# Kernel optimization log

Hardware: AMD Instinct MI355X
Metric: run time of the kernel (lower is better)

## Reference

```python
import jax, jax.numpy as jnp
import numpy as np

D_MODEL = 1024
N_HEADS = 16
HEAD_DIM = D_MODEL // N_HEADS
D_FF = 4096
LN_EPS = 1e-5


def _layer_norm(x, gamma, beta):
    mu = jnp.mean(x, axis=-1, keepdims=True)
    var = jnp.var(x, axis=-1, keepdims=True)
    return (x - mu) * jax.lax.rsqrt(var + LN_EPS) * gamma + beta


def setup_inputs() -> dict:
    key = jax.random.key(0)
    ks = jax.random.split(key, 16)
    s = 1.0 / np.sqrt(D_MODEL)
    sf = 1.0 / np.sqrt(D_FF)
    return {
        "x": jax.random.normal(ks[0], (4, 2048, D_MODEL), dtype=jnp.float32),
        "w_q": jax.random.uniform(ks[1], (D_MODEL, D_MODEL), jnp.float32, -s, s),
        "b_q": jax.random.uniform(ks[2], (D_MODEL,), jnp.float32, -s, s),
        "w_k": jax.random.uniform(ks[3], (D_MODEL, D_MODEL), jnp.float32, -s, s),
        "b_k": jax.random.uniform(ks[4], (D_MODEL,), jnp.float32, -s, s),
        "w_v": jax.random.uniform(ks[5], (D_MODEL, D_MODEL), jnp.float32, -s, s),
        "b_v": jax.random.uniform(ks[6], (D_MODEL,), jnp.float32, -s, s),
        "w_o": jax.random.uniform(ks[7], (D_MODEL, D_MODEL), jnp.float32, -s, s),
        "b_o": jax.random.uniform(ks[8], (D_MODEL,), jnp.float32, -s, s),
        "ln1_g": jnp.ones((D_MODEL,), jnp.float32),
        "ln1_b": jnp.zeros((D_MODEL,), jnp.float32),
        "w1": jax.random.uniform(ks[9], (D_MODEL, D_FF), jnp.float32, -s, s),
        "b1": jax.random.uniform(ks[10], (D_FF,), jnp.float32, -s, s),
        "w2": jax.random.uniform(ks[11], (D_FF, D_MODEL), jnp.float32, -sf, sf),
        "b2": jax.random.uniform(ks[12], (D_MODEL,), jnp.float32, -sf, sf),
        "ln2_g": jnp.ones((D_MODEL,), jnp.float32),
        "ln2_b": jnp.zeros((D_MODEL,), jnp.float32),
    }


def reference(x, w_q, b_q, w_k, b_k, w_v, b_v, w_o, b_o,
              ln1_g, ln1_b, w1, b1, w2, b2, ln2_g, ln2_b):
    B, S, D = x.shape
    # projections -> [B, H, S, Hd]
    def split_heads(t):
        return t.reshape(B, S, N_HEADS, HEAD_DIM).transpose(0, 2, 1, 3)
    q = split_heads(x @ w_q + b_q)
    k = split_heads(x @ w_k + b_k)
    v = split_heads(x @ w_v + b_v)
    scale = jnp.float32(np.sqrt(HEAD_DIM))
    scores = jnp.einsum('bhqd,bhkd->bhqk', q, k) / scale
    attn = jax.nn.softmax(scores, axis=-1)  # dropout = identity in eval
    ctx = jnp.einsum('bhqk,bhkd->bhqd', attn, v)
    ctx = ctx.transpose(0, 2, 1, 3).reshape(B, S, D)
    attn_out = ctx @ w_o + b_o
    h = _layer_norm(x + attn_out, ln1_g, ln1_b)
    ffn = jax.nn.relu(h @ w1 + b1) @ w2 + b2
    return _layer_norm(h + ffn, ln2_g, ln2_b)
```

## Files before the change

kernel.cpp:

```cpp
#include <hip/hip_runtime.h>
#include <cstdint>
#include <cstddef>

typedef unsigned short u16;
typedef short s16x8 __attribute__((ext_vector_type(8)));
typedef unsigned short u16x8 __attribute__((ext_vector_type(8)));
typedef unsigned short u16x4 __attribute__((ext_vector_type(4)));
typedef float f32x4 __attribute__((ext_vector_type(4)));
typedef unsigned int u32x2 __attribute__((ext_vector_type(2)));

#define MFMA_BF16(a, b, c) __builtin_amdgcn_mfma_f32_16x16x32_bf16((a), (b), (c), 0, 0, 0)

__device__ __forceinline__ float b2f(u16 u) {
    union { unsigned int i; float f; } x;
    x.i = ((unsigned int)u) << 16;
    return x.f;
}
__device__ __forceinline__ u16 f2b(float f) {
    union { float f; unsigned int i; } x;
    x.f = f;
    return (u16)((x.i + 0x8000u) >> 16);
}
__device__ __forceinline__ float exp2_hw(float x) {
    float r;
    asm volatile("v_exp_f32 %0, %1" : "=v"(r) : "v"(x));
    return r;
}
__device__ __forceinline__ unsigned int cvt_pk_bf16(float lo, float hi) {
    unsigned int r;
    asm("v_cvt_pk_bf16_f32 %0, %1, %2" : "=v"(r) : "v"(lo), "v"(hi));
    return r;
}

__device__ __forceinline__ void gload_lds16(const u16* g, u16* l) {
    __builtin_amdgcn_global_load_lds((__attribute__((address_space(1))) void*)(g),
                                     (__attribute__((address_space(3))) void*)(l),
                                     16, 0, 0);
}

__device__ __forceinline__ void transpose_tile(const float* __restrict__ in,
                                               u16* __restrict__ out,
                                               int R, int C, int bx, int by) {
    __shared__ u16 t[64][68];
    const int tc = bx * 64, tr = by * 64;
    for (int i = 0; i < 16; i++) {
        int idx = threadIdx.x + i * 256;
        int r = idx >> 6, c = idx & 63;
        t[r][c] = f2b(in[(size_t)(tr + r) * C + tc + c]);
    }
    __syncthreads();
    for (int i = 0; i < 16; i++) {
        int idx = threadIdx.x + i * 256;
        int r = idx >> 6, c = idx & 63;
        out[(size_t)(tc + r) * R + tr + c] = t[c][r];
    }
}

__global__ __launch_bounds__(256)
void prep_all(const float* __restrict__ w_q, const float* __restrict__ w_k,
              const float* __restrict__ w_v, const float* __restrict__ w_o,
              const float* __restrict__ w1, const float* __restrict__ w2,
              const float* __restrict__ x,
              u16* __restrict__ wqkv_t, u16* __restrict__ wo_t,
              u16* __restrict__ w1_t, u16* __restrict__ w2_t,
              u16* __restrict__ x_bf) {
    const int id = blockIdx.x;
    if (id < 1024) {
        const int j = id >> 8, lid = id & 255;
        const float* in = (j == 0) ? w_q : (j == 1) ? w_k : (j == 2) ? w_v : w_o;
        u16* out = (j == 0) ? wqkv_t
                 : (j == 1) ? wqkv_t + 1024 * 1024
                 : (j == 2) ? wqkv_t + 2 * 1024 * 1024
                 : wo_t;
        transpose_tile(in, out, 1024, 1024, lid & 15, lid >> 4);
    } else if (id < 2048) {
        const int lid = id - 1024;
        transpose_tile(w1, w1_t, 1024, 4096, lid & 63, lid >> 6);
    } else if (id < 3072) {
        const int lid = id - 2048;
        transpose_tile(w2, w2_t, 4096, 1024, lid & 15, lid >> 4);
    } else {
        const int i = ((id - 3072) * 256 + threadIdx.x) * 8;
        float4 a = *(const float4*)(x + i);
        float4 b = *(const float4*)(x + i + 4);
        u16x8 o;
        o[0] = f2b(a.x); o[1] = f2b(a.y); o[2] = f2b(a.z); o[3] = f2b(a.w);
        o[4] = f2b(b.x); o[5] = f2b(b.y); o[6] = f2b(b.z); o[7] = f2b(b.w);
        *(u16x8*)(x_bf + i) = o;
    }
}

enum { EPI_PLAIN = 0, EPI_RELU = 1, EPI_QKV = 2 };
#define SC_QK 0.1803368801111204f

template <int EPI>
__global__ __launch_bounds__(256, 3)
void gemm_bt(const u16* __restrict__ A, const u16* __restrict__ Bt,
             const float* __restrict__ bias0, const float* __restrict__ bias1,
             const float* __restrict__ bias2,
             u16* __restrict__ C0, u16* __restrict__ C1, u16* __restrict__ C2,
             int M, int N, int K) {
    __shared__ u16 As[128 * 64];
    __shared__ u16 Bs[128 * 64];
    const int tid = threadIdx.x;
    const int lane = tid & 63;
    const int wave = tid >> 6;
    const int qd = lane >> 4, cl = lane & 15;
    const int wr = (wave >> 1) * 64, wc = (wave & 1) * 64;
    const int m0 = blockIdx.x * 128, n0 = blockIdx.y * 128;

    const u16* AgP[4];
    const u16* BgP[4];
    int dsto[4];
    for (int c = 0; c < 4; c++) {
        const int d = tid * 8 + c * 2048;
        const int row = d >> 6;
        const int sblk = ((d >> 3) & 7) ^ (row & 7);
        AgP[c] = A + (size_t)(m0 + row) * K + sblk * 8;
        BgP[c] = Bt + (size_t)(n0 + row) * K + sblk * 8;
        dsto[c] = d;
    }

    const f32x4 Z = {0.f, 0.f, 0.f, 0.f};
    f32x4 acc[4][4];
    for (int i = 0; i < 4; i++)
        for (int j = 0; j < 4; j++) acc[i][j] = Z;

    for (int k = 0; k < K; k += 64) {
        __syncthreads();
        for (int c = 0; c < 4; c++) {
            gload_lds16(AgP[c] + k, As + dsto[c]);
            gload_lds16(BgP[c] + k, Bs + dsto[c]);
        }
        __syncthreads();
        for (int kk = 0; kk < 2; kk++) {
            s16x8 af[4], bfr[4];
            for (int i = 0; i < 4; i++) {
                const int row = wr + i * 16 + cl;
                af[i] = *(const s16x8*)(As + row * 64 +
                                        (((kk << 2) | qd) ^ (row & 7)) * 8);
            }
            for (int j = 0; j < 4; j++) {
                const int row = wc + j * 16 + cl;
                bfr[j] = *(const s16x8*)(Bs + row * 64 +
                                         (((kk << 2) | qd) ^ (row & 7)) * 8);
            }
            for (int i = 0; i < 4; i++)
                for (int j = 0; j < 4; j++)
                    acc[i][j] = MFMA_BF16(af[i], bfr[j], acc[i][j]);
        }
    }

    for (int j = 0; j < 4; j++) {
        const int col = n0 + wc + j * 16 + cl;
        float bv;
        if (EPI == EPI_QKV) {
            const int t = col >> 10, nn = col & 1023;
            const float* bp = (t == 0) ? bias0 : ((t == 1) ? bias1 : bias2);
            bv = bp[nn];
        } else {
            bv = bias0[col];
        }
        if (EPI == EPI_QKV && (col >> 10) == 2) {
            const int nn = col & 1023;
            const int hh = nn >> 6, d = nn & 63;
            for (int i = 0; i < 4; i++) {
                const int row0 = m0 + wr + i * 16 + qd * 4;
                const int b = row0 >> 11, s = row0 & 2047;
                const int bh = b * 16 + hh;
                u16x4 pk;
                for (int r = 0; r < 4; r++) pk[r] = f2b(acc[i][j][r] + bv);
                *(u16x4*)(&C2[((size_t)bh * 64 + d) * 2048 + s]) = pk;
            }
        } else {
            for (int i = 0; i < 4; i++) {
                for (int r = 0; r < 4; r++) {
                    const int row = m0 + wr + i * 16 + qd * 4 + r;
                    float v = acc[i][j][r] + bv;
                    if (EPI == EPI_RELU) v = fmaxf(v, 0.f);
                    if (EPI == EPI_QKV) {
                        const int t = col >> 10, nn = col & 1023;
                        const int hh = nn >> 6, d = nn & 63;
                        const int b = row >> 11, s = row & 2047;
                        const int bh = b * 16 + hh;
                        if (t == 0)
                            C0[((size_t)bh * 2048 + s) * 64 + d] = f2b(v * SC_QK);
                        else
                            C1[((size_t)bh * 2048 + s) * 64 + d] = f2b(v);
                    } else {
                        C0[(size_t)row * N + col] = f2b(v);
                    }
                }
            }
        }
    }
}

__global__ __launch_bounds__(256)
void flash_attn(const u16* __restrict__ Q, const u16* __restrict__ K,
                const u16* __restrict__ Vt, u16* __restrict__ ctx) {
    __shared__ u16 Ks[2][64 * 64];
    __shared__ u16 Vs[2][64 * 64];
    __shared__ u16 Ps[4][32 * 72];
    const int tid = threadIdx.x, lane = tid & 63, wave = tid >> 6;
    const int qd = lane >> 4, cl = lane & 15;
    const int bh = blockIdx.x;
    const int s0 = blockIdx.y * 128 + wave * 32;

    const u16* Kb = K + (size_t)bh * 2048 * 64;
    const u16* Vb = Vt + (size_t)bh * 64 * 2048;

    const int e0 = tid, e1 = tid + 256;
    const int r0 = e0 >> 3, bb0 = (e0 & 7) ^ (r0 & 7);
    const int r1 = e1 >> 3, bb1 = (e1 & 7) ^ (r1 & 7);

    gload_lds16(Kb + (size_t)r0 * 64 + bb0 * 8, &Ks[0][e0 * 8]);
    gload_lds16(Kb + (size_t)r1 * 64 + bb1 * 8, &Ks[0][e1 * 8]);
    gload_lds16(Vb + (size_t)r0 * 2048 + bb0 * 8, &Vs[0][e0 * 8]);
    gload_lds16(Vb + (size_t)r1 * 2048 + bb1 * 8, &Vs[0][e1 * 8]);

    const u16* Qb = Q + ((size_t)bh * 2048 + s0) * 64;
    s16x8 qf[2][2];
    for (int m = 0; m < 2; m++) {
        qf[m][0] = *(const s16x8*)(Qb + (m * 16 + cl) * 64 + qd * 8);
        qf[m][1] = *(const s16x8*)(Qb + (m * 16 + cl) * 64 + 32 + qd * 8);
    }

    s16x8 onesf;
    for (int i = 0; i < 8; i++) onesf[i] = (short)0x3F80;

    const f32x4 Z = {0.f, 0.f, 0.f, 0.f};
    f32x4 o_acc[2][4], l_acc[2];
    for (int m = 0; m < 2; m++) {
        l_acc[m] = Z;
        for (int t = 0; t < 4; t++) o_acc[m][t] = Z;
    }

    u16* pw = &Ps[wave][0];
    __syncthreads();

    for (int kb = 0; kb < 32; kb++) {
        const int cur = kb & 1;
        if (kb < 31) {
            const int kn = kb + 1;
            gload_lds16(Kb + (size_t)(kn * 64 + r0) * 64 + bb0 * 8, &Ks[cur ^ 1][e0 * 8]);
            gload_lds16(Kb + (size_t)(kn * 64 + r1) * 64 + bb1 * 8, &Ks[cur ^ 1][e1 * 8]);
            gload_lds16(Vb + (size_t)r0 * 2048 + kn * 64 + bb0 * 8, &Vs[cur ^ 1][e0 * 8]);
            gload_lds16(Vb + (size_t)r1 * 2048 + kn * 64 + bb1 * 8, &Vs[cur ^ 1][e1 * 8]);
        }
        const u16* ks = Ks[cur];
        const u16* vs = Vs[cur];

        f32x4 sacc[2][4];
        for (int m = 0; m < 2; m++)
            for (int t = 0; t < 4; t++) sacc[m][t] = Z;
        for (int t = 0; t < 4; t++) {
            const int row = t * 16 + cl;
            s16x8 kf0 = *(const s16x8*)(ks + row * 64 + (qd ^ (row & 7)) * 8);
            s16x8 kf1 = *(const s16x8*)(ks + row * 64 + ((qd + 4) ^ (row & 7)) * 8);
            for (int m = 0; m < 2; m++) {
                sacc[m][t] = MFMA_BF16(kf0, qf[m][0], sacc[m][t]);
                sacc[m][t] = MFMA_BF16(kf1, qf[m][1], sacc[m][t]);
            }
        }

        for (int m = 0; m < 2; m++)
            for (int t = 0; t < 4; t++) {
                const float p0 = exp2_hw(sacc[m][t][0]);
                const float p1 = exp2_hw(sacc[m][t][1]);
                const float p2 = exp2_hw(sacc[m][t][2]);
                const float p3 = exp2_hw(sacc[m][t][3]);
                u32x2 w;
                w[0] = cvt_pk_bf16(p0, p1);
                w[1] = cvt_pk_bf16(p2, p3);
                *(u32x2*)(pw + (m * 16 + cl) * 72 + t * 16 + qd * 4) = w;
            }

        for (int kk = 0; kk < 2; kk++) {
            s16x8 vf[4];
            for (int t = 0; t < 4; t++) {
                const int row = t * 16 + cl;
                vf[t] = *(const s16x8*)(vs + row * 64 +
                                        ((kk * 4 + qd) ^ (row & 7)) * 8);
            }
            for (int m = 0; m < 2; m++) {
                s16x8 pf = *(const s16x8*)(pw + (m * 16 + cl) * 72 + kk * 32 + qd * 8);
                for (int t = 0; t < 4; t++)
                    o_acc[m][t] = MFMA_BF16(vf[t], pf, o_acc[m][t]);
                l_acc[m] = MFMA_BF16(onesf, pf, l_acc[m]);
            }
        }
        __syncthreads();
    }

    const int b = bh >> 4, hh = bh & 15;
    for (int m = 0; m < 2; m++) {
        const float inv = 1.f / l_acc[m][0];
        const int s = s0 + m * 16 + cl;
        u16* cp = ctx + ((size_t)(b * 2048 + s)) * 1024 + hh * 64 + qd * 4;
        for (int t = 0; t < 4; t++) {
            u16x4 pk;
            for (int r = 0; r < 4; r++) pk[r] = f2b(o_acc[m][t][r] * inv);
            *(u16x4*)(cp + t * 16) = pk;
        }
    }
}

template <int MODE>
__global__ __launch_bounds__(256)
void ln_res(const void* __restrict__ Xv, const u16* __restrict__ Y,
            const float* __restrict__ G, const float* __restrict__ Bp,
            void* __restrict__ Ov) {
    const int row = blockIdx.x * 4 + (threadIdx.x >> 6);
    const int lane = threadIdx.x & 63;
    const int off = lane * 16;
    float v[16];
    float s = 0.f, s2 = 0.f;
    const u16* y = Y + (size_t)row * 1024 + off;
    if (MODE == 0) {
        const float* X = (const float*)Xv + (size_t)row * 1024 + off;
        for (int i = 0; i < 2; i++) {
            float4 xa = *(const float4*)(X + i * 8);
            float4 xb = *(const float4*)(X + i * 8 + 4);
            u16x8 yv = *(const u16x8*)(y + i * 8);
            float xs[8] = {xa.x, xa.y, xa.z, xa.w, xb.x, xb.y, xb.z, xb.w};
            for (int j = 0; j < 8; j++) {
                const float t = xs[j] + b2f(yv[j]);
                v[i * 8 + j] = t;
                s += t;
                s2 += t * t;
            }
        }
    } else {
        const u16* X = (const u16*)Xv + (size_t)row * 1024 + off;
        for (int i = 0; i < 2; i++) {
            u16x8 xv = *(const u16x8*)(X + i * 8);
            u16x8 yv = *(const u16x8*)(y + i * 8);
            for (int j = 0; j < 8; j++) {
                const float t = b2f(xv[j]) + b2f(yv[j]);
                v[i * 8 + j] = t;
                s += t;
                s2 += t * t;
            }
        }
    }
    for (int o = 32; o >= 1; o >>= 1) {
        s += __shfl_xor(s, o, 64);
        s2 += __shfl_xor(s2, o, 64);
    }
    const float mu = s * (1.f / 1024.f);
    const float var = s2 * (1.f / 1024.f) - mu * mu;
    const float rs = rsqrtf(var + 1e-5f);
    const float* g = G + off;
    const float* bp = Bp + off;
    for (int i = 0; i < 2; i++) {
        float4 ga = *(const float4*)(g + i * 8);
        float4 gb = *(const float4*)(g + i * 8 + 4);
        float4 ba = *(const float4*)(bp + i * 8);
        float4 bb = *(const float4*)(bp + i * 8 + 4);
        float gs[8] = {ga.x, ga.y, ga.z, ga.w, gb.x, gb.y, gb.z, gb.w};
        float bs[8] = {ba.x, ba.y, ba.z, ba.w, bb.x, bb.y, bb.z, bb.w};
        if (MODE == 0) {
            u16* o = (u16*)Ov + (size_t)row * 1024 + off;
            u16x8 ov;
            for (int j = 0; j < 8; j++)
                ov[j] = f2b((v[i * 8 + j] - mu) * rs * gs[j] + bs[j]);
            *(u16x8*)(o + i * 8) = ov;
        } else {
            float* o = (float*)Ov + (size_t)row * 1024 + off;
            float4 o0, o1;
            o0.x = (v[i * 8 + 0] - mu) * rs * gs[0] + bs[0];
            o0.y = (v[i * 8 + 1] - mu) * rs * gs[1] + bs[1];
            o0.z = (v[i * 8 + 2] - mu) * rs * gs[2] + bs[2];
            o0.w = (v[i * 8 + 3] - mu) * rs * gs[3] + bs[3];
            o1.x = (v[i * 8 + 4] - mu) * rs * gs[4] + bs[4];
            o1.y = (v[i * 8 + 5] - mu) * rs * gs[5] + bs[5];
            o1.z = (v[i * 8 + 6] - mu) * rs * gs[6] + bs[6];
            o1.w = (v[i * 8 + 7] - mu) * rs * gs[7] + bs[7];
            *(float4*)(o + i * 8) = o0;
            *(float4*)(o + i * 8 + 4) = o1;
        }
    }
}

extern "C" void kernel_launch(void* const* d_in, const int* in_sizes, int n_in,
                              void* d_out, int out_size, void* d_ws, size_t ws_size,
                              hipStream_t stream) {
    const float* x    = (const float*)d_in[0];
    const float* w_q  = (const float*)d_in[1];
    const float* b_q  = (const float*)d_in[2];
    const float* w_k  = (const float*)d_in[3];
    const float* b_k  = (const float*)d_in[4];
    const float* w_v  = (const float*)d_in[5];
    const float* b_v  = (const float*)d_in[6];
    const float* w_o  = (const float*)d_in[7];
    const float* b_o  = (const float*)d_in[8];
    const float* ln1g = (const float*)d_in[9];
    const float* ln1b = (const float*)d_in[10];
    const float* w1   = (const float*)d_in[11];
    const float* b1   = (const float*)d_in[12];
    const float* w2   = (const float*)d_in[13];
    const float* b2   = (const float*)d_in[14];
    const float* ln2g = (const float*)d_in[15];
    const float* ln2b = (const float*)d_in[16];
    float* out = (float*)d_out;

    char* ws = (char*)d_ws;
    const size_t MB = 1024 * 1024;
    u16* wqkv_t = (u16*)(ws + 0);
    u16* wo_t   = (u16*)(ws + 6 * MB);
    u16* w1_t   = (u16*)(ws + 8 * MB);
    u16* w2_t   = (u16*)(ws + 16 * MB);
    u16* x_bf   = (u16*)(ws + 24 * MB);
    u16* Qs     = (u16*)(ws + 40 * MB);
    u16* Kk     = (u16*)(ws + 56 * MB);
    u16* Vt     = (u16*)(ws + 72 * MB);
    u16* ctx    = (u16*)(ws + 88 * MB);
    u16* attn   = (u16*)(ws + 104 * MB);
    u16* h      = attn;
    u16* ffn1   = (u16*)(ws + 24 * MB);
    u16* ffn2   = (u16*)(ws + 88 * MB);

    prep_all<<<7168, 256, 0, stream>>>(w_q, w_k, w_v, w_o, w1, w2, x,
                                       wqkv_t, wo_t, w1_t, w2_t, x_bf);

    gemm_bt<EPI_QKV><<<dim3(64, 24), 256, 0, stream>>>(
        x_bf, wqkv_t, b_q, b_k, b_v, Qs, Kk, Vt, 8192, 3072, 1024);

    flash_attn<<<dim3(64, 16), 256, 0, stream>>>(Qs, Kk, Vt, ctx);

    gemm_bt<EPI_PLAIN><<<dim3(64, 8), 256, 0, stream>>>(
        ctx, wo_t, b_o, nullptr, nullptr, attn, nullptr, nullptr, 8192, 1024, 1024);

    ln_res<0><<<2048, 256, 0, stream>>>(x, attn, ln1g, ln1b, h);

    gemm_bt<EPI_RELU><<<dim3(64, 32), 256, 0, stream>>>(
        h, w1_t, b1, nullptr, nullptr, ffn1, nullptr, nullptr, 8192, 4096, 1024);
    gemm_bt<EPI_PLAIN><<<dim3(64, 8), 256, 0, stream>>>(
        ffn1, w2_t, b2, nullptr, nullptr, ffn2, nullptr, nullptr, 8192, 1024, 4096);

    ln_res<1><<<2048, 256, 0, stream>>>(h, ffn2, ln2g, ln2b, out);

    (void)in_sizes; (void)n_in; (void)out_size; (void)ws_size;
}
```

Baseline: 511.2 us.

## Redistribute attention probabilities with permlane swaps instead of LDS round-trip

The flash attention kernel no longer writes the exponentiated score tile to a per-wave LDS buffer and reads it back in PV operand layout. It now rearranges the packed bf16 values in registers with v_permlane32_swap and v_permlane16_swap, which removes the LDS stores and loads and frees shared memory. It also unrolls the key-block loop by two so the buffer indices are constants, and wraps the MFMA phases in s_setprio to favour matrix work. The lane permutation has to produce exactly the layout the old LDS transpose did, otherwise the results will be wrong.

```diff
diff --git a/kernel.cpp b/kernel.cpp
--- a/kernel.cpp
+++ b/kernel.cpp
@@ -7,7 +7,9 @@
 typedef unsigned short u16x8 __attribute__((ext_vector_type(8)));
 typedef unsigned short u16x4 __attribute__((ext_vector_type(4)));
 typedef float f32x4 __attribute__((ext_vector_type(4)));
+typedef unsigned int u32;
 typedef unsigned int u32x2 __attribute__((ext_vector_type(2)));
+typedef unsigned int u32x4 __attribute__((ext_vector_type(4)));
 
 #define MFMA_BF16(a, b, c) __builtin_amdgcn_mfma_f32_16x16x32_bf16((a), (b), (c), 0, 0, 0)
 
@@ -201,7 +203,6 @@
                 const u16* __restrict__ Vt, u16* __restrict__ ctx) {
     __shared__ u16 Ks[2][64 * 64];
     __shared__ u16 Vs[2][64 * 64];
-    __shared__ u16 Ps[4][32 * 72];
     const int tid = threadIdx.x, lane = tid & 63, wave = tid >> 6;
     const int qd = lane >> 4, cl = lane & 15;
     const int bh = blockIdx.x;
@@ -236,62 +237,81 @@
         for (int t = 0; t < 4; t++) o_acc[m][t] = Z;
     }
 
-    u16* pw = &Ps[wave][0];
     __syncthreads();
 
-    for (int kb = 0; kb < 32; kb++) {
-        const int cur = kb & 1;
-        if (kb < 31) {
-            const int kn = kb + 1;
-            gload_lds16(Kb + (size_t)(kn * 64 + r0) * 64 + bb0 * 8, &Ks[cur ^ 1][e0 * 8]);
-            gload_lds16(Kb + (size_t)(kn * 64 + r1) * 64 + bb1 * 8, &Ks[cur ^ 1][e1 * 8]);
-            gload_lds16(Vb + (size_t)r0 * 2048 + kn * 64 + bb0 * 8, &Vs[cur ^ 1][e0 * 8]);
-            gload_lds16(Vb + (size_t)r1 * 2048 + kn * 64 + bb1 * 8, &Vs[cur ^ 1][e1 * 8]);
-        }
-        const u16* ks = Ks[cur];
-        const u16* vs = Vs[cur];
-
-        f32x4 sacc[2][4];
-        for (int m = 0; m < 2; m++)
-            for (int t = 0; t < 4; t++) sacc[m][t] = Z;
-        for (int t = 0; t < 4; t++) {
-            const int row = t * 16 + cl;
-            s16x8 kf0 = *(const s16x8*)(ks + row * 64 + (qd ^ (row & 7)) * 8);
-            s16x8 kf1 = *(const s16x8*)(ks + row * 64 + ((qd + 4) ^ (row & 7)) * 8);
-            for (int m = 0; m < 2; m++) {
-                sacc[m][t] = MFMA_BF16(kf0, qf[m][0], sacc[m][t]);
-                sacc[m][t] = MFMA_BF16(kf1, qf[m][1], sacc[m][t]);
-            }
-        }
-
-        for (int m = 0; m < 2; m++)
-            for (int t = 0; t < 4; t++) {
-                const float p0 = exp2_hw(sacc[m][t][0]);
-                const float p1 = exp2_hw(sacc[m][t][1]);
-                const float p2 = exp2_hw(sacc[m][t][2]);
-                const float p3 = exp2_hw(sacc[m][t][3]);
-                u32x2 w;
-                w[0] = cvt_pk_bf16(p0, p1);
-                w[1] = cvt_pk_bf16(p2, p3);
-                *(u32x2*)(pw + (m * 16 + cl) * 72 + t * 16 + qd * 4) = w;
-            }
-
-        for (int kk = 0; kk < 2; kk++) {
-            s16x8 vf[4];
-            for (int t = 0; t < 4; t++) {
-                const int row = t * 16 + cl;
-                vf[t] = *(const s16x8*)(vs + row * 64 +
-                                        ((kk * 4 + qd) ^ (row & 7)) * 8);
-            }
-            for (int m = 0; m < 2; m++) {
-                s16x8 pf = *(const s16x8*)(pw + (m * 16 + cl) * 72 + kk * 32 + qd * 8);
-                for (int t = 0; t < 4; t++)
-                    o_acc[m][t] = MFMA_BF16(vf[t], pf, o_acc[m][t]);
-                l_acc[m] = MFMA_BF16(onesf, pf, l_acc[m]);
-            }
-        }
-        __syncthreads();
-    }
+#define ATTN_ITER(CUR, KB, DO_STAGE)                                           \
+    {                                                                          \
+        if (DO_STAGE) {                                                        \
+            const int kn = (KB) + 1;                                           \
+            gload_lds16(Kb + (size_t)(kn * 64 + r0) * 64 + bb0 * 8,            \
+                        &Ks[(CUR) ^ 1][e0 * 8]);                               \
+            gload_lds16(Kb + (size_t)(kn * 64 + r1) * 64 + bb1 * 8,            \
+                        &Ks[(CUR) ^ 1][e1 * 8]);                               \
+            gload_lds16(Vb + (size_t)r0 * 2048 + kn * 64 + bb0 * 8,            \
+                        &Vs[(CUR) ^ 1][e0 * 8]);                               \
+            gload_lds16(Vb + (size_t)r1 * 2048 + kn * 64 + bb1 * 8,            \
+                        &Vs[(CUR) ^ 1][e1 * 8]);                               \
+        }                                                                      \
+        const u16* ks = Ks[CUR];                                               \
+        const u16* vs = Vs[CUR];                                               \
+        f32x4 sacc[2][4];                                                      \
+        for (int m = 0; m < 2; m++)                                            \
+            for (int t = 0; t < 4; t++) sacc[m][t] = Z;                        \
+        __builtin_amdgcn_s_setprio(1);                                         \
+        for (int t = 0; t < 4; t++) {                                          \
+            const int row = t * 16 + cl;                                       \
+            s16x8 kf0 = *(const s16x8*)(ks + row * 64 + (qd ^ (row & 7)) * 8); \
+            s16x8 kf1 = *(const s16x8*)(ks + row * 64 +                        \
+                                        ((qd + 4) ^ (row & 7)) * 8);           \
+            for (int m = 0; m < 2; m++) {                                      \
+                sacc[m][t] = MFMA_BF16(kf0, qf[m][0], sacc[m][t]);             \
+                sacc[m][t] = MFMA_BF16(kf1, qf[m][1], sacc[m][t]);             \
+            }                                                                  \
+        }                                                                      \
+        __builtin_amdgcn_s_setprio(0);                                         \
+        u32x2 w[2][4];                                                         \
+        for (int m = 0; m < 2; m++)                                            \
+            for (int t = 0; t < 4; t++) {                                      \
+                const float p0 = exp2_hw(sacc[m][t][0]);                       \
+                const float p1 = exp2_hw(sacc[m][t][1]);                       \
+                const float p2 = exp2_hw(sacc[m][t][2]);                       \
+                const float p3 = exp2_hw(sacc[m][t][3]);                       \
+                w[m][t][0] = cvt_pk_bf16(p0, p1);                              \
+                w[m][t][1] = cvt_pk_bf16(p2, p3);                              \
+            }                                                                  \
+        __builtin_amdgcn_s_setprio(1);                                         \
+        for (int kk = 0; kk < 2; kk++) {                                       \
+            s16x8 vf[4];                                                       \
+            for (int t = 0; t < 4; t++) {                                      \
+                const int row = t * 16 + cl;                                   \
+                vf[t] = *(const s16x8*)(vs + row * 64 +                        \
+                                        ((kk * 4 + qd) ^ (row & 7)) * 8);      \
+            }                                                                  \
+            for (int m = 0; m < 2; m++) {                                      \
+                union { u32x4 u; s16x8 s; } pfu;                               \
+                for (int c = 0; c < 2; c++) {                                  \
+                    u32 a = w[m][2 * kk][c];                                   \
+                    u32 b = w[m][2 * kk + 1][c];                               \
+                    asm("v_permlane32_swap_b32 %0, %1" : "+v"(a), "+v"(b));    \
+                    asm("v_permlane16_swap_b32 %0, %1" : "+v"(a), "+v"(b));    \
+                    pfu.u[c] = a;                                              \
+                    pfu.u[2 + c] = b;                                          \
+                }                                                              \
+                const s16x8 pf = pfu.s;                                        \
+                for (int t = 0; t < 4; t++)                                    \
+                    o_acc[m][t] = MFMA_BF16(vf[t], pf, o_acc[m][t]);           \
+                l_acc[m] = MFMA_BF16(onesf, pf, l_acc[m]);                     \
+            }                                                                  \
+        }                                                                      \
+        __builtin_amdgcn_s_setprio(0);                                         \
+        __syncthreads();                                                       \
+    }
+
+    for (int j = 0; j < 16; j++) {
+        ATTN_ITER(0, 2 * j, true);
+        ATTN_ITER(1, 2 * j + 1, (j < 15));
+    }
+#undef ATTN_ITER
 
     const int b = bh >> 4, hh = bh & 15;
     for (int m = 0; m < 2; m++) {
```

Result: faster. 476.1 us, median of 2 (-6.8%).
